# Optimization experiments

Hardware: AMD Instinct MI355X
Metric: run time of the kernel (lower is better)

## Reference

```python
import jax, jax.numpy as jnp
import numpy as np

LENS = 0.5
GAMMA = 0.5
B_J0 = 0.1
BETA = 1.8

@jax.custom_vjp
def spike(x):
    return (x > 0).astype(x.dtype)

def _gauss(x, mu, sigma):
    return jnp.exp(-(x - mu) ** 2 / (2.0 * sigma ** 2)) / jnp.sqrt(2.0 * jnp.pi) / sigma

def _spike_fwd(x):
    return spike(x), x

def _spike_bwd(x, g):
    scale, hight = 6.0, 0.15
    temp = (_gauss(x, 0.0, LENS) * (1.0 + hight)
            - _gauss(x, LENS, scale * LENS) * hight
            - _gauss(x, -LENS, scale * LENS) * hight)
    return (g * temp * GAMMA,)

spike.defvjp(_spike_fwd, _spike_bwd)

CFG_FC = [512, 512, 512]
IN_SIZE = 1024
OUT_SIZE = 11

def setup_inputs() -> dict:
    key = jax.random.key(0)
    ks = jax.random.split(key, 20)
    def xavier(k, shape):
        fan_in, fan_out = shape[1], shape[0]
        lim = np.sqrt(6.0 / (fan_in + fan_out))
        return jax.random.uniform(k, shape, jnp.float32, -lim, lim)
    x = jax.random.normal(ks[0], (64, 100, 2, 128, 128), jnp.float32)
    w_i2h1 = xavier(ks[1], (CFG_FC[0], IN_SIZE)); b_i2h1 = jnp.zeros((CFG_FC[0],), jnp.float32)
    w_i2h2 = xavier(ks[2], (CFG_FC[1], IN_SIZE)); b_i2h2 = jnp.zeros((CFG_FC[1],), jnp.float32)
    w_i2h3 = xavier(ks[3], (CFG_FC[2], CFG_FC[0] + CFG_FC[1])); b_i2h3 = jnp.zeros((CFG_FC[2],), jnp.float32)
    # orthogonal init for h2h_3
    a = jax.random.normal(ks[4], (CFG_FC[2], CFG_FC[2]), jnp.float32)
    q, _ = jnp.linalg.qr(a)
    w_h2h3 = q; b_h2h3 = jnp.zeros((CFG_FC[2],), jnp.float32)
    w_h2o3 = xavier(ks[5], (OUT_SIZE, CFG_FC[2])); b_h2o3 = jnp.zeros((OUT_SIZE,), jnp.float32)
    tau_adp_h1 = 200.0 + 50.0 * jax.random.normal(ks[6], (CFG_FC[0],), jnp.float32)
    tau_adp_h2 = 200.0 + 50.0 * jax.random.normal(ks[7], (CFG_FC[1],), jnp.float32)
    tau_adp_h3 = 200.0 + 50.0 * jax.random.normal(ks[8], (CFG_FC[2],), jnp.float32)
    tau_m_h1 = 20.0 + 5.0 * jax.random.normal(ks[9], (CFG_FC[0],), jnp.float32)
    tau_m_h2 = 20.0 + 5.0 * jax.random.normal(ks[10], (CFG_FC[1],), jnp.float32)
    tau_m_h3 = 20.0 + 5.0 * jax.random.normal(ks[11], (CFG_FC[2],), jnp.float32)
    return dict(x=x, w_i2h1=w_i2h1, b_i2h1=b_i2h1, w_i2h2=w_i2h2, b_i2h2=b_i2h2,
                w_i2h3=w_i2h3, b_i2h3=b_i2h3, w_h2h3=w_h2h3, b_h2h3=b_h2h3,
                w_h2o3=w_h2o3, b_h2o3=b_h2o3,
                tau_adp_h1=tau_adp_h1, tau_adp_h2=tau_adp_h2, tau_adp_h3=tau_adp_h3,
                tau_m_h1=tau_m_h1, tau_m_h2=tau_m_h2, tau_m_h3=tau_m_h3)

def _alif_update(inp, mem, spk, bb, alpha, ro):
    # adaptive LIF neuron update (mem_update_adp with isAdapt=1)
    bb = ro * bb + (1.0 - ro) * spk
    B = B_J0 + BETA * bb
    mem = mem * alpha + (1.0 - alpha) * inp - B * spk
    spk = spike(mem - B)
    return mem, spk, bb

def reference(x, w_i2h1, b_i2h1, w_i2h2, b_i2h2, w_i2h3, b_i2h3,
              w_h2h3, b_h2h3, w_h2o3, b_h2o3,
              tau_adp_h1, tau_adp_h2, tau_adp_h3,
              tau_m_h1, tau_m_h2, tau_m_h3):
    N, T, C, H, W = x.shape
    h1, h2, h3 = w_i2h1.shape[0], w_i2h2.shape[0], w_h2h3.shape[0]
    # max_pool2d(k=4, s=4), vectorized over all timesteps at once
    xp = x.reshape(N, T, C, H // 4, 4, W // 4, 4).max(axis=(4, 6))
    xp = xp.reshape(N, T, C, (H // 4) * (W // 4))  # [N,T,C,input_size]
    # precompute feedforward projections for all timesteps: [T,N,h]
    in1 = jnp.einsum('nti,hi->tnh', xp[:, :, 0], w_i2h1) + b_i2h1
    in2 = jnp.einsum('nti,hi->tnh', xp[:, :, 1], w_i2h2) + b_i2h2
    alpha1 = jnp.exp(-1.0 / tau_m_h1); ro1 = jnp.exp(-1.0 / tau_adp_h1)
    alpha2 = jnp.exp(-1.0 / tau_m_h2); ro2 = jnp.exp(-1.0 / tau_adp_h2)
    alpha3 = jnp.exp(-1.0 / tau_m_h3); ro3 = jnp.exp(-1.0 / tau_adp_h3)

    def step(carry, ins):
        m1, s1, b1, m2, s2, b2, m3, s3, b3 = carry
        i1, i2 = ins
        m1, s1, b1 = _alif_update(i1, m1, s1, b1, alpha1, ro1)
        m2, s2, b2 = _alif_update(i2, m2, s2, b2, alpha2, ro2)
        # dropout layers run in eval mode (identity)
        h3_in = (jnp.concatenate([s1, s2], axis=-1) @ w_i2h3.T + b_i2h3
                 + s3 @ w_h2h3.T + b_h2h3)
        m3, s3, b3 = _alif_update(h3_in, m3, s3, b3, alpha3, ro3)
        return (m1, s1, b1, m2, s2, b2, m3, s3, b3), None

    z = lambda d: jnp.zeros((N, d), x.dtype)
    bj = lambda d: jnp.full((N, d), B_J0, x.dtype)
    carry0 = (z(h1), z(h1), bj(h1), z(h2), z(h2), bj(h2), z(h3), z(h3), bj(h3))
    carry, _ = jax.lax.scan(step, carry0, (in1, in2))
    s3_final = carry[7]
    return s3_final @ w_h2o3.T + b_h2o3  # [N, out_size]
```

## Files before the change

kernel.cpp:

```cpp
#include <hip/hip_runtime.h>
#include <cstdint>
#include <cstddef>

#define B_J0 0.1f
#define BETA 1.8f

__global__ __launch_bounds__(256) void maxpool_kernel(
    const float* __restrict__ x, float* __restrict__ xp1, float* __restrict__ xp2)
{
    int tid = blockIdx.x * blockDim.x + threadIdx.x;
    int p   = tid & 1023;
    int ntc = tid >> 10;
    int c   = ntc & 1;
    int nt  = ntc >> 1;
    int t   = nt % 100;
    int n   = nt / 100;
    int ph = p >> 5, pw = p & 31;
    const float* base = x + (size_t)ntc * 16384 + (size_t)(ph * 4) * 128 + pw * 4;
    float4 v0 = *(const float4*)(base);
    float m = fmaxf(fmaxf(v0.x, v0.y), fmaxf(v0.z, v0.w));
#pragma unroll
    for (int r = 1; r < 4; ++r) {
        float4 v = *(const float4*)(base + r * 128);
        m = fmaxf(m, fmaxf(fmaxf(v.x, v.y), fmaxf(v.z, v.w)));
    }
    float* dst = c ? xp2 : xp1;
    dst[(size_t)(t * 64 + n) * 1024 + p] = m;
}

__global__ __launch_bounds__(256) void transpose512(
    const float* __restrict__ w, float* __restrict__ wT)
{
    int tid = blockIdx.x * blockDim.x + threadIdx.x;
    int h = tid & 511, k = tid >> 9;
    wT[tid] = w[h * 512 + k];
}

__global__ __launch_bounds__(256) void gemm_abt(
    const float* __restrict__ A0, const float* __restrict__ A1,
    const float* __restrict__ B0, const float* __restrict__ B1,
    const float* __restrict__ bias0, const float* __restrict__ bias1,
    float* __restrict__ C, int ldc, int colStride)
{
    const int K = 1024;
    int mt = blockIdx.x;
    int nt = blockIdx.y;
    int c  = blockIdx.z;
    const float* A    = c ? A1 : A0;
    const float* B    = c ? B1 : B0;
    const float* bias = c ? bias1 : bias0;

    __shared__ float As[16][128];
    __shared__ float Bs[16][64];

    int tid = threadIdx.x;
    int tx = tid & 15;
    int ty = tid >> 4;

    float acc[8][4] = {};
    const float* Ab = A + (size_t)mt * 128 * K;
    const float* Bb = B + (size_t)nt * 64 * K;

    for (int k0 = 0; k0 < K; k0 += 16) {
#pragma unroll
        for (int i = 0; i < 2; ++i) {
            int fid = i * 256 + tid;
            int k4 = fid & 3, row = fid >> 2;
            float4 v = *(const float4*)(Ab + (size_t)row * K + k0 + k4 * 4);
            As[k4 * 4 + 0][row] = v.x; As[k4 * 4 + 1][row] = v.y;
            As[k4 * 4 + 2][row] = v.z; As[k4 * 4 + 3][row] = v.w;
        }
        {
            int fid = tid;
            int k4 = fid & 3, row = fid >> 2;
            float4 v = *(const float4*)(Bb + (size_t)row * K + k0 + k4 * 4);
            Bs[k4 * 4 + 0][row] = v.x; Bs[k4 * 4 + 1][row] = v.y;
            Bs[k4 * 4 + 2][row] = v.z; Bs[k4 * 4 + 3][row] = v.w;
        }
        __syncthreads();
#pragma unroll
        for (int kk = 0; kk < 16; ++kk) {
            float a[8], b[4];
            *(float4*)&a[0] = *(const float4*)&As[kk][ty * 8];
            *(float4*)&a[4] = *(const float4*)&As[kk][ty * 8 + 4];
            *(float4*)&b[0] = *(const float4*)&Bs[kk][tx * 4];
#pragma unroll
            for (int i = 0; i < 8; ++i)
#pragma unroll
                for (int j = 0; j < 4; ++j)
                    acc[i][j] += a[i] * b[j];
        }
        __syncthreads();
    }

    int nc = nt * 64 + tx * 4;
    int colbase = c * colStride + nc;
    float4 bv = *(const float4*)(bias + nc);
#pragma unroll
    for (int i = 0; i < 8; ++i) {
        int row = mt * 128 + ty * 8 + i;
        float4 o;
        o.x = acc[i][0] + bv.x;
        o.y = acc[i][1] + bv.y;
        o.z = acc[i][2] + bv.z;
        o.w = acc[i][3] + bv.w;
        *(float4*)(C + (size_t)row * ldc + colbase) = o;
    }
}

__global__ __launch_bounds__(256) void alif12_kernel(
    const float* __restrict__ in12, float* __restrict__ spk12,
    const float* __restrict__ tau_m1, const float* __restrict__ tau_adp1,
    const float* __restrict__ tau_m2, const float* __restrict__ tau_adp2)
{
    int tid = blockIdx.x * blockDim.x + threadIdx.x;
    int col = tid & 1023;
    int n   = tid >> 10;
    int c = col >> 9, h = col & 511;
    float tm = c ? tau_m2[h] : tau_m1[h];
    float ta = c ? tau_adp2[h] : tau_adp1[h];
    float alpha = expf(-1.0f / tm);
    float ro    = expf(-1.0f / ta);
    float m = 0.f, s = 0.f, b = B_J0;
    for (int t = 0; t < 100; ++t) {
        size_t idx = (size_t)(t * 64 + n) * 1024 + col;
        float inp = in12[idx];
        b = ro * b + (1.f - ro) * s;
        float Bv = B_J0 + BETA * b;
        m = m * alpha + (1.f - alpha) * inp - Bv * s;
        s = (m - Bv) > 0.f ? 1.f : 0.f;
        spk12[idx] = s;
    }
}

__global__ __launch_bounds__(512) void scan3_kernel(
    const float* __restrict__ ff3, const float* __restrict__ wT,
    const float* __restrict__ b_h2h3,
    const float* __restrict__ tau_m3, const float* __restrict__ tau_adp3,
    const float* __restrict__ w_h2o3, const float* __restrict__ b_h2o3,
    float* __restrict__ out)
{
    __shared__ int   act[512];
    __shared__ int   cnts[8];
    __shared__ float part[11 * 8];

    int n = blockIdx.x;
    int h = threadIdx.x;
    int lane = h & 63, wid = h >> 6;

    float alpha = expf(-1.0f / tau_m3[h]);
    float ro    = expf(-1.0f / tau_adp3[h]);
    float bh    = b_h2h3[h];
    const float* wcol = wT + h;

    float m = 0.f, s = 0.f, b = B_J0;
    int total = 0;

    for (int t = 0; t < 100; ++t) {
        float acc = ff3[(size_t)(t * 64 + n) * 512 + h] + bh;
        int j = 0;
        for (; j + 3 < total; j += 4) {
            int k0 = act[j], k1 = act[j + 1], k2 = act[j + 2], k3 = act[j + 3];
            float w0 = wcol[(size_t)k0 * 512];
            float w1 = wcol[(size_t)k1 * 512];
            float w2 = wcol[(size_t)k2 * 512];
            float w3 = wcol[(size_t)k3 * 512];
            acc += w0; acc += w1; acc += w2; acc += w3;
        }
        for (; j < total; ++j) acc += wcol[(size_t)act[j] * 512];

        b = ro * b + (1.f - ro) * s;
        float Bv = B_J0 + BETA * b;
        m = m * alpha + (1.f - alpha) * acc - Bv * s;
        s = (m - Bv) > 0.f ? 1.f : 0.f;

        __syncthreads();
        unsigned long long ball = __ballot(s > 0.f);
        if (lane == 0) cnts[wid] = __popcll(ball);
        __syncthreads();
        int newtotal = 0, myoff = 0;
#pragma unroll
        for (int w = 0; w < 8; ++w) {
            int cw = cnts[w];
            if (w < wid) myoff += cw;
            newtotal += cw;
        }
        if (s > 0.f) {
            int lp = __popcll(ball & ((1ull << lane) - 1ull));
            act[myoff + lp] = h;
        }
        total = newtotal;
        __syncthreads();
    }

#pragma unroll 1
    for (int o = 0; o < 11; ++o) {
        float v = (s > 0.f) ? w_h2o3[o * 512 + h] : 0.f;
#pragma unroll
        for (int offs = 32; offs > 0; offs >>= 1) v += __shfl_down(v, offs);
        if (lane == 0) part[o * 8 + wid] = v;
    }
    __syncthreads();
    if (h < 11) {
        float r = 0.f;
#pragma unroll
        for (int w = 0; w < 8; ++w) r += part[h * 8 + w];
        out[n * 11 + h] = r + b_h2o3[h];
    }
}

extern "C" void kernel_launch(void* const* d_in, const int* in_sizes, int n_in,
                              void* d_out, int out_size, void* d_ws, size_t ws_size,
                              hipStream_t stream)
{
    const float* x        = (const float*)d_in[0];
    const float* w_i2h1   = (const float*)d_in[1];
    const float* b_i2h1   = (const float*)d_in[2];
    const float* w_i2h2   = (const float*)d_in[3];
    const float* b_i2h2   = (const float*)d_in[4];
    const float* w_i2h3   = (const float*)d_in[5];
    const float* b_i2h3   = (const float*)d_in[6];
    const float* w_h2h3   = (const float*)d_in[7];
    const float* b_h2h3   = (const float*)d_in[8];
    const float* w_h2o3   = (const float*)d_in[9];
    const float* b_h2o3   = (const float*)d_in[10];
    const float* tau_adp1 = (const float*)d_in[11];
    const float* tau_adp2 = (const float*)d_in[12];
    const float* tau_adp3 = (const float*)d_in[13];
    const float* tau_m1   = (const float*)d_in[14];
    const float* tau_m2   = (const float*)d_in[15];
    const float* tau_m3   = (const float*)d_in[16];
    float* out = (float*)d_out;
    float* ws  = (float*)d_ws;

    float* xp1   = ws;
    float* xp2   = ws + 6553600;
    float* in12  = ws + 13107200;
    float* wT    = ws + 19660800;
    float* spk12 = xp1;
    float* ff3   = xp2;

    maxpool_kernel<<<dim3(51200), dim3(256), 0, stream>>>(x, xp1, xp2);
    transpose512<<<dim3(1024), dim3(256), 0, stream>>>(w_h2h3, wT);
    gemm_abt<<<dim3(50, 8, 2), dim3(256), 0, stream>>>(
        xp1, xp2, w_i2h1, w_i2h2, b_i2h1, b_i2h2, in12, 1024, 512);
    alif12_kernel<<<dim3(256), dim3(256), 0, stream>>>(
        in12, spk12, tau_m1, tau_adp1, tau_m2, tau_adp2);
    gemm_abt<<<dim3(50, 8, 1), dim3(256), 0, stream>>>(
        spk12, nullptr, w_i2h3, nullptr, b_i2h3, nullptr, ff3, 512, 0);
    scan3_kernel<<<dim3(64), dim3(512), 0, stream>>>(
        ff3, wT, b_h2h3, tau_m3, tau_adp3, w_h2o3, b_h2o3, out);
}
```

Before: 1.534 ms.

## Replace sparse recurrent spike gather with 8-bit subset-sum lookup table

Precomputes, for every group of 8 presynaptic neurons and every 256-value spike mask, the summed recurrent weights per output neuron. The layer-3 scan then does a fixed 64 table lookups per step indexed by spike bitmasks instead of walking a variable-length active list. The block doubles to 1024 threads so the two halves split the groups, and the compaction phase is replaced by ballot words. It adds a 32 MB table build and a larger L2 working set, and the summation order changes slightly.

```diff
diff --git a/kernel.cpp b/kernel.cpp
--- a/kernel.cpp
+++ b/kernel.cpp
@@ -34,6 +34,24 @@
     int tid = blockIdx.x * blockDim.x + threadIdx.x;
     int h = tid & 511, k = tid >> 9;
     wT[tid] = w[h * 512 + k];
+}
+
+__global__ __launch_bounds__(256) void build_table(
+    const float* __restrict__ wT, float* __restrict__ tbl)
+{
+    int g = blockIdx.x;
+    int h = blockIdx.y * 256 + threadIdx.x;
+    float w[8];
+#pragma unroll
+    for (int b = 0; b < 8; ++b) w[b] = wT[(size_t)(g * 8 + b) * 512 + h];
+    float* dst = tbl + ((size_t)g << 8) * 512 + h;
+    for (int mask = 0; mask < 256; ++mask) {
+        float sacc = 0.f;
+#pragma unroll
+        for (int b = 0; b < 8; ++b)
+            if (mask & (1 << b)) sacc += w[b];
+        dst[(size_t)mask * 512] = sacc;
+    }
 }
 
 __global__ __launch_bounds__(256) void gemm_abt(
@@ -133,63 +151,70 @@
     }
 }
 
-__global__ __launch_bounds__(512) void scan3_kernel(
-    const float* __restrict__ ff3, const float* __restrict__ wT,
+__global__ __launch_bounds__(1024) void scan3_kernel(
+    const float* __restrict__ ff3, const float* __restrict__ tbl,
     const float* __restrict__ b_h2h3,
     const float* __restrict__ tau_m3, const float* __restrict__ tau_adp3,
     const float* __restrict__ w_h2o3, const float* __restrict__ b_h2o3,
     float* __restrict__ out)
 {
-    __shared__ int   act[512];
-    __shared__ int   cnts[8];
-    __shared__ float part[11 * 8];
-
-    int n = blockIdx.x;
-    int h = threadIdx.x;
-    int lane = h & 63, wid = h >> 6;
+    __shared__ unsigned int bwords[16];
+    __shared__ float pacc[512];
+    __shared__ float part[11 * 16];
+
+    int tid  = threadIdx.x;
+    int half = tid >> 9;
+    int h    = tid & 511;
+    int n    = blockIdx.x;
+    int lane = tid & 63, wid = tid >> 6;
 
     float alpha = expf(-1.0f / tau_m3[h]);
     float ro    = expf(-1.0f / tau_adp3[h]);
     float bh    = b_h2h3[h];
-    const float* wcol = wT + h;
+    const float* tcol = tbl + h;
+    int gbase = half * 32;
 
     float m = 0.f, s = 0.f, b = B_J0;
-    int total = 0;
+    if (tid < 16) bwords[tid] = 0u;
+    __syncthreads();
 
     for (int t = 0; t < 100; ++t) {
-        float acc = ff3[(size_t)(t * 64 + n) * 512 + h] + bh;
-        int j = 0;
-        for (; j + 3 < total; j += 4) {
-            int k0 = act[j], k1 = act[j + 1], k2 = act[j + 2], k3 = act[j + 3];
-            float w0 = wcol[(size_t)k0 * 512];
-            float w1 = wcol[(size_t)k1 * 512];
-            float w2 = wcol[(size_t)k2 * 512];
-            float w3 = wcol[(size_t)k3 * 512];
-            acc += w0; acc += w1; acc += w2; acc += w3;
-        }
-        for (; j < total; ++j) acc += wcol[(size_t)act[j] * 512];
-
-        b = ro * b + (1.f - ro) * s;
-        float Bv = B_J0 + BETA * b;
-        m = m * alpha + (1.f - alpha) * acc - Bv * s;
-        s = (m - Bv) > 0.f ? 1.f : 0.f;
-
-        __syncthreads();
-        unsigned long long ball = __ballot(s > 0.f);
-        if (lane == 0) cnts[wid] = __popcll(ball);
-        __syncthreads();
-        int newtotal = 0, myoff = 0;
-#pragma unroll
-        for (int w = 0; w < 8; ++w) {
-            int cw = cnts[w];
-            if (w < wid) myoff += cw;
-            newtotal += cw;
-        }
-        if (s > 0.f) {
-            int lp = __popcll(ball & ((1ull << lane) - 1ull));
-            act[myoff + lp] = h;
-        }
-        total = newtotal;
+        float ff = (half == 0) ? ff3[(size_t)(t * 64 + n) * 512 + h] : 0.f;
+
+        unsigned int bw[8];
+#pragma unroll
+        for (int i = 0; i < 8; ++i) bw[i] = bwords[gbase / 4 + i];
+
+        float wv[32];
+#pragma unroll
+        for (int gl = 0; gl < 32; ++gl) {
+            unsigned msk = (bw[gl >> 2] >> ((gl & 3) * 8)) & 0xFFu;
+            unsigned idx = (((unsigned)(gbase + gl) << 8) | msk) * 512u;
+            wv[gl] = tcol[idx];
+        }
+        float a0 = 0.f, a1 = 0.f, a2 = 0.f, a3 = 0.f;
+        float a4 = 0.f, a5 = 0.f, a6 = 0.f, a7 = 0.f;
+#pragma unroll
+        for (int gl = 0; gl < 32; gl += 8) {
+            a0 += wv[gl + 0]; a1 += wv[gl + 1]; a2 += wv[gl + 2]; a3 += wv[gl + 3];
+            a4 += wv[gl + 4]; a5 += wv[gl + 5]; a6 += wv[gl + 6]; a7 += wv[gl + 7];
+        }
+        float gsum = ((a0 + a1) + (a2 + a3)) + ((a4 + a5) + (a6 + a7));
+        if (half == 1) pacc[h] = gsum;
+        __syncthreads();
+
+        if (half == 0) {
+            float acc = (ff + bh) + gsum + pacc[h];
+            b = ro * b + (1.f - ro) * s;
+            float Bv = B_J0 + BETA * b;
+            m = m * alpha + (1.f - alpha) * acc - Bv * s;
+            s = (m - Bv) > 0.f ? 1.f : 0.f;
+            unsigned long long ball = __ballot(s > 0.f);
+            if (lane == 0) {
+                bwords[wid * 2]     = (unsigned)(ball & 0xFFFFFFFFull);
+                bwords[wid * 2 + 1] = (unsigned)(ball >> 32);
+            }
+        }
         __syncthreads();
     }
 
@@ -198,14 +223,14 @@
         float v = (s > 0.f) ? w_h2o3[o * 512 + h] : 0.f;
 #pragma unroll
         for (int offs = 32; offs > 0; offs >>= 1) v += __shfl_down(v, offs);
-        if (lane == 0) part[o * 8 + wid] = v;
+        if (lane == 0) part[o * 16 + wid] = v;
     }
     __syncthreads();
-    if (h < 11) {
+    if (tid < 11) {
         float r = 0.f;
 #pragma unroll
-        for (int w = 0; w < 8; ++w) r += part[h * 8 + w];
-        out[n * 11 + h] = r + b_h2o3[h];
+        for (int w = 0; w < 16; ++w) r += part[tid * 16 + w];
+        out[n * 11 + tid] = r + b_h2o3[tid];
     }
 }
 
@@ -237,17 +262,19 @@
     float* xp2   = ws + 6553600;
     float* in12  = ws + 13107200;
     float* wT    = ws + 19660800;
+    float* tbl   = ws + 19922944;
     float* spk12 = xp1;
     float* ff3   = xp2;
 
     maxpool_kernel<<<dim3(51200), dim3(256), 0, stream>>>(x, xp1, xp2);
     transpose512<<<dim3(1024), dim3(256), 0, stream>>>(w_h2h3, wT);
+    build_table<<<dim3(64, 2), dim3(256), 0, stream>>>(wT, tbl);
     gemm_abt<<<dim3(50, 8, 2), dim3(256), 0, stream>>>(
         xp1, xp2, w_i2h1, w_i2h2, b_i2h1, b_i2h2, in12, 1024, 512);
     alif12_kernel<<<dim3(256), dim3(256), 0, stream>>>(
         in12, spk12, tau_m1, tau_adp1, tau_m2, tau_adp2);
     gemm_abt<<<dim3(50, 8, 1), dim3(256), 0, stream>>>(
         spk12, nullptr, w_i2h3, nullptr, b_i2h3, nullptr, ff3, 512, 0);
-    scan3_kernel<<<dim3(64), dim3(512), 0, stream>>>(
-        ff3, wT, b_h2h3, tau_m3, tau_adp3, w_h2o3, b_h2o3, out);
-}
+    scan3_kernel<<<dim3(64), dim3(1024), 0, stream>>>(
+        ff3, tbl, b_h2h3, tau_m3, tau_adp3, w_h2o3, b_h2o3, out);
+}
```

Result: slower. 1.620 ms (+5.6%).
